# Kernel optimization log

Hardware: AMD Instinct MI355X
Metric: run time of the kernel (lower is better)

## Reference

```python
import jax, jax.numpy as jnp
import numpy as np

N_NODES = 100000
N_EDGES = 6400000


def setup_inputs() -> dict:
    key = jax.random.key(0)
    k = jax.random.split(key, 5)
    x = jax.random.normal(k[0], (N_NODES, 4), dtype=jnp.float32)
    edge_index = jax.random.randint(k[1], (2, N_EDGES), 0, N_NODES, dtype=jnp.int32)
    # Glorot-style init for GCN linear weights
    W1 = jax.random.normal(k[2], (4, 16), dtype=jnp.float32) * (1.0 / np.sqrt(4.0))
    b1 = jnp.zeros((16,), dtype=jnp.float32)
    W2 = jax.random.normal(k[3], (16, 2), dtype=jnp.float32) * (1.0 / np.sqrt(16.0))
    b2 = jnp.zeros((2,), dtype=jnp.float32)
    return {"x": x, "edge_index": edge_index, "W1": W1, "b1": b1, "W2": W2, "b2": b2}


def _gcn_conv(x, src, dst, deg_inv_sqrt, W, b):
    """One GCNConv layer: linear transform -> symmetric-normalized scatter-add -> bias.

    src, dst already include self-loops; deg_inv_sqrt precomputed on the
    self-loop-augmented graph (matches PyG GCNConv defaults).
    """
    n = x.shape[0]
    h = x @ W                                   # [N, F_out]
    coef = deg_inv_sqrt[src] * deg_inv_sqrt[dst]  # [E+N]
    msg = h[src] * coef[:, None]                # gather + scale, [E+N, F_out]
    out = jax.ops.segment_sum(msg, dst, num_segments=n)  # scatter-add
    return out + b


def reference(x, edge_index, W1, b1, W2, b2):
    n = x.shape[0]
    loop = jnp.arange(n, dtype=edge_index.dtype)
    src = jnp.concatenate([edge_index[0], loop])  # add self-loops
    dst = jnp.concatenate([edge_index[1], loop])
    deg = jax.ops.segment_sum(jnp.ones_like(dst, dtype=x.dtype), dst, num_segments=n)
    deg_inv_sqrt = jnp.where(deg > 0, jax.lax.rsqrt(deg), 0.0)

    h = jax.nn.relu(_gcn_conv(x, src, dst, deg_inv_sqrt, W1, b1))
    return _gcn_conv(h, src, dst, deg_inv_sqrt, W2, b2)
```

## Files before the change

kernel.cpp:

```cpp
#include <hip/hip_runtime.h>

#define TPB 256
#define CSH 10
#define CN 1024
#define NBC_MAX 128
#define STILE 8192
#define EPT (STILE / TPB)

#define P2 16
#define P2_SH 4
#define SB_SH 8
#define SBN_MAX 512

#define B20 1048576
#define S1F 131072.0f
#define S2F 8192.0f

typedef unsigned long long u64;

__device__ __forceinline__ unsigned enc_fx(float v, float scale) {
    int xi = __float2int_rn(v * scale);
    xi = max(-(B20 - 1), min(B20 - 1, xi));
    return (unsigned)(xi + B20);
}

__global__ void k_zero2(int* __restrict__ a, int na, int* __restrict__ b, int nb) {
    int i = blockIdx.x * blockDim.x + threadIdx.x;
    if (i < na) a[i] = 0;
    if (i < nb) b[i] = 0;
}

__global__ void k_hist0(const int* __restrict__ dst, int* __restrict__ hist0,
                        int NBC, int E) {
    __shared__ int hh[NBC_MAX];
    for (int i = threadIdx.x; i < NBC_MAX; i += TPB) hh[i] = 0;
    __syncthreads();
    int stride = gridDim.x * blockDim.x;
    for (int i = blockIdx.x * blockDim.x + threadIdx.x; i < E; i += stride)
        atomicAdd(&hh[dst[i] >> CSH], 1);
    __syncthreads();
    for (int i = threadIdx.x; i < NBC; i += TPB)
        if (hh[i]) atomicAdd(&hist0[i], hh[i]);
}

__global__ void k_scanbase(const int* __restrict__ bsize, int* __restrict__ base,
                           int* __restrict__ cur, int NBC) {
    __shared__ int s[NBC_MAX];
    int t = threadIdx.x;
    if (t < NBC_MAX) s[t] = (t < NBC) ? bsize[t] : 0;
    __syncthreads();
    for (int off = 1; off < NBC_MAX; off <<= 1) {
        int v = 0;
        if (t < NBC_MAX && t >= off) v = s[t - off];
        __syncthreads();
        if (t < NBC_MAX) s[t] += v;
        __syncthreads();
    }
    if (t < NBC) {
        int b = (t == 0) ? 0 : s[t - 1];
        base[t] = b;
        cur[t] = b;
    }
    if (t == 0) base[NBC] = s[NBC - 1];
}

__global__ void k_bscat(const int* __restrict__ src, const int* __restrict__ dst,
                        int* __restrict__ cur, unsigned* __restrict__ packed,
                        int E, int NBC) {
    __shared__ unsigned stage[STILE];
    __shared__ int cnt[NBC_MAX], lb[NBC_MAX], resv[NBC_MAX];
    int tb = blockIdx.x * STILE;
    int te = min(E, tb + STILE);
    if (threadIdx.x < NBC_MAX) cnt[threadIdx.x] = 0;
    __syncthreads();
    unsigned pk[EPT];
    int br[EPT];
#pragma unroll
    for (int u = 0; u < EPT; u++) {
        int i = tb + u * TPB + (int)threadIdx.x;
        br[u] = -1;
        if (i < te) {
            int d = dst[i];
            int b = d >> CSH;
            pk[u] = ((unsigned)src[i] << CSH) | (unsigned)(d & (CN - 1));
            int r = atomicAdd(&cnt[b], 1);
            br[u] = b | (r << 7);
        }
    }
    __syncthreads();
    if (threadIdx.x < (unsigned)NBC) {
        int b = threadIdx.x;
        int sum = 0;
        for (int j = 0; j < b; j++) sum += cnt[j];
        lb[b] = sum;
        resv[b] = cnt[b] ? atomicAdd(&cur[b], cnt[b]) : 0;
    }
    __syncthreads();
#pragma unroll
    for (int u = 0; u < EPT; u++) {
        if (br[u] >= 0) {
            int b = br[u] & (NBC_MAX - 1);
            stage[lb[b] + (br[u] >> 7)] = pk[u];
        }
    }
    __syncthreads();
    int wv = threadIdx.x >> 6, lane = threadIdx.x & 63;
    for (int b = wv; b < NBC; b += 4) {
        int c = cnt[b];
        if (!c) continue;
        int gb = resv[b], s0 = lb[b];
        for (int i = lane; i < c; i += 64)
            packed[gb + i] = stage[s0 + i];
    }
}

__global__ void k_p2hist(const unsigned* __restrict__ packed, const int* __restrict__ base,
                         int* __restrict__ h, int* __restrict__ deg, int SBN, int N) {
    __shared__ int hsb[SBN_MAX];
    __shared__ int dcnt[CN];
    int b = blockIdx.x >> P2_SH, p = blockIdx.x & (P2 - 1);
    for (int i = threadIdx.x; i < SBN_MAX; i += TPB) hsb[i] = 0;
    for (int i = threadIdx.x; i < CN; i += TPB) dcnt[i] = 0;
    __syncthreads();
    int lo = base[b], sz = base[b + 1] - lo;
    int i0 = lo + (int)((long long)sz * p / P2);
    int i1 = lo + (int)((long long)sz * (p + 1) / P2);
    int a0 = min(i1, (i0 + 3) & ~3);
    int a1 = a0 + ((i1 - a0) & ~3);
    for (int i = i0 + (int)threadIdx.x; i < a0; i += TPB) {
        unsigned pk = packed[i];
        atomicAdd(&hsb[pk >> (CSH + SB_SH)], 1);
        atomicAdd(&dcnt[pk & (CN - 1)], 1);
    }
    for (int i = a0 + (int)threadIdx.x * 4; i < a1; i += TPB * 4) {
        uint4 q = *(const uint4*)(packed + i);
        atomicAdd(&hsb[q.x >> (CSH + SB_SH)], 1); atomicAdd(&dcnt[q.x & (CN - 1)], 1);
        atomicAdd(&hsb[q.y >> (CSH + SB_SH)], 1); atomicAdd(&dcnt[q.y & (CN - 1)], 1);
        atomicAdd(&hsb[q.z >> (CSH + SB_SH)], 1); atomicAdd(&dcnt[q.z & (CN - 1)], 1);
        atomicAdd(&hsb[q.w >> (CSH + SB_SH)], 1); atomicAdd(&dcnt[q.w & (CN - 1)], 1);
    }
    for (int i = a1 + (int)threadIdx.x; i < i1; i += TPB) {
        unsigned pk = packed[i];
        atomicAdd(&hsb[pk >> (CSH + SB_SH)], 1);
        atomicAdd(&dcnt[pk & (CN - 1)], 1);
    }
    __syncthreads();
    int* hp = h + (size_t)blockIdx.x * SBN;
    for (int i2 = threadIdx.x; i2 < SBN; i2 += TPB) hp[i2] = hsb[i2];
    int node0 = b << CSH;
    for (int i2 = threadIdx.x; i2 < CN; i2 += TPB)
        if (dcnt[i2] && node0 + i2 < N) atomicAdd(&deg[node0 + i2], dcnt[i2]);
}

__global__ void k_scan3(int* __restrict__ h, const int* __restrict__ base, int SBN) {
    __shared__ int tsum[TPB];
    int b = blockIdx.x;
    int* hb = h + (size_t)b * P2 * SBN;
    int n = SBN * P2;
    int per = (n + TPB - 1) / TPB;
    int i0 = threadIdx.x * per;
    int vals[32];
    int sum = 0;
    for (int k = 0; k < per && k < 32; k++) {
        int idx = i0 + k;
        int v = 0;
        if (idx < n) {
            int sb = idx >> P2_SH, p = idx & (P2 - 1);
            v = hb[p * SBN + sb];
        }
        vals[k] = v;
        sum += v;
    }
    tsum[threadIdx.x] = sum;
    __syncthreads();
    for (int off = 1; off < TPB; off <<= 1) {
        int v = (threadIdx.x >= off) ? tsum[threadIdx.x - off] : 0;
        __syncthreads();
        tsum[threadIdx.x] += v;
        __syncthreads();
    }
    int run = base[b] + ((threadIdx.x == 0) ? 0 : tsum[threadIdx.x - 1]);
    for (int k = 0; k < per && k < 32; k++) {
        int idx = i0 + k;
        if (idx < n) {
            int sb = idx >> P2_SH, p = idx & (P2 - 1);
            hb[p * SBN + sb] = run;
            run += vals[k];
        }
    }
}

__global__ void k_p2scat(const unsigned* __restrict__ packed, const int* __restrict__ base,
                         const int* __restrict__ h, unsigned* __restrict__ packed2,
                         int SBN) {
    __shared__ int goff[SBN_MAX];
    __shared__ int cnt2[SBN_MAX];
    int b = blockIdx.x >> P2_SH, p = blockIdx.x & (P2 - 1);
    const int* hp = h + (size_t)blockIdx.x * SBN;
    for (int i = threadIdx.x; i < SBN_MAX; i += TPB) {
        cnt2[i] = 0;
        goff[i] = (i < SBN) ? hp[i] : 0;
    }
    __syncthreads();
    int lo = base[b], sz = base[b + 1] - lo;
    int i0 = lo + (int)((long long)sz * p / P2);
    int i1 = lo + (int)((long long)sz * (p + 1) / P2);
    int a0 = min(i1, (i0 + 3) & ~3);
    int a1 = a0 + ((i1 - a0) & ~3);
    for (int i = i0 + (int)threadIdx.x; i < a0; i += TPB) {
        unsigned pk = packed[i];
        int sb2 = pk >> (CSH + SB_SH);
        int r = atomicAdd(&cnt2[sb2], 1);
        packed2[goff[sb2] + r] = pk;
    }
    for (int i = a0 + (int)threadIdx.x * 4; i < a1; i += TPB * 4) {
        uint4 q = *(const uint4*)(packed + i);
        int sa = q.x >> (CSH + SB_SH), sb_ = q.y >> (CSH + SB_SH);
        int sc = q.z >> (CSH + SB_SH), sd = q.w >> (CSH + SB_SH);
        int ra = atomicAdd(&cnt2[sa], 1);
        int rb = atomicAdd(&cnt2[sb_], 1);
        int rc = atomicAdd(&cnt2[sc], 1);
        int rd = atomicAdd(&cnt2[sd], 1);
        packed2[goff[sa] + ra] = q.x;
        packed2[goff[sb_] + rb] = q.y;
        packed2[goff[sc] + rc] = q.z;
        packed2[goff[sd] + rd] = q.w;
    }
    for (int i = a1 + (int)threadIdx.x; i < i1; i += TPB) {
        unsigned pk = packed[i];
        int sb2 = pk >> (CSH + SB_SH);
        int r = atomicAdd(&cnt2[sb2], 1);
        packed2[goff[sb2] + r] = pk;
    }
}

__global__ void k_prepv(const float* __restrict__ x, const int* __restrict__ deg,
                        float* __restrict__ xs, unsigned* __restrict__ xse, int N) {
    int v = blockIdx.x * blockDim.x + threadIdx.x;
    if (v >= N) return;
    float di = rsqrtf((float)(deg[v] + 1));
    float4 xv = ((const float4*)x)[v];
    xv.x *= di; xv.y *= di; xv.z *= di; xv.w *= di;
    ((float4*)xs)[v] = xv;
    uint4 e;
    e.x = enc_fx(xv.x, S1F); e.y = enc_fx(xv.y, S1F);
    e.z = enc_fx(xv.z, S1F); e.w = enc_fx(xv.w, S1F);
    ((uint4*)xse)[v] = e;
}

#define AGG1_AT(pkv, gv) { int n_ = (int)((pkv) & (CN - 1)) * 3; \
    atomicAdd(&acc[n_],     (u64)(gv).x | ((u64)(gv).y << 32)); \
    atomicAdd(&acc[n_ + 1], (u64)(gv).z | ((u64)(gv).w << 32)); }

__global__ void k_agg1n(const unsigned* __restrict__ packed2, const int* __restrict__ base,
                        const unsigned* __restrict__ xse, u64* __restrict__ partial1, int S1) {
    __shared__ u64 acc[CN * 3];
    for (int i = threadIdx.x; i < CN * 3; i += TPB) acc[i] = 0ULL;
    __syncthreads();
    int b = blockIdx.x / S1, s = blockIdx.x - b * S1;
    int lo = base[b], sz = base[b + 1] - lo;
    int i0 = lo + (int)((long long)sz * s / S1);
    int i1 = lo + (int)((long long)sz * (s + 1) / S1);
    const uint4* xse4 = (const uint4*)xse;
    int i = i0 + (int)threadIdx.x;
    for (; i + 3 * TPB < i1; i += 4 * TPB) {
        unsigned pa = packed2[i];
        unsigned pb = packed2[i + TPB];
        unsigned pc = packed2[i + 2 * TPB];
        unsigned pd = packed2[i + 3 * TPB];
        uint4 ga = xse4[pa >> CSH];
        uint4 gb = xse4[pb >> CSH];
        uint4 gc = xse4[pc >> CSH];
        uint4 gd = xse4[pd >> CSH];
        AGG1_AT(pa, ga); AGG1_AT(pb, gb); AGG1_AT(pc, gc); AGG1_AT(pd, gd);
    }
    for (; i < i1; i += TPB) {
        unsigned pk = packed2[i];
        uint4 g = xse4[pk >> CSH];
        AGG1_AT(pk, g);
    }
    __syncthreads();
    u64* p = partial1 + (size_t)blockIdx.x * (CN * 2);
    for (int i2 = threadIdx.x; i2 < CN * 2; i2 += TPB)
        p[i2] = acc[(i2 >> 1) * 3 + (i2 & 1)];
}

__global__ void k_comb1q(const u64* __restrict__ partial1,
                         const float* __restrict__ xs, const int* __restrict__ deg,
                         const float* __restrict__ W1, const float* __restrict__ b1,
                         const float* __restrict__ W2,
                         float* __restrict__ hs2f, unsigned* __restrict__ hs2e,
                         int S1, int N) {
    __shared__ float w1[64], w2[32], bb[16];
    if (threadIdx.x < 64) w1[threadIdx.x] = W1[threadIdx.x];
    if (threadIdx.x < 32) w2[threadIdx.x] = W2[threadIdx.x];
    if (threadIdx.x < 16) bb[threadIdx.x] = b1[threadIdx.x];
    __syncthreads();
    int v = blockIdx.x * blockDim.x + threadIdx.x;
    if (v >= N) return;
    int b = v >> CSH, lv = v & (CN - 1);
    u64 a01 = 0, a23 = 0;
    for (int s = 0; s < S1; s++) {
        const u64* q = partial1 + ((size_t)(b * S1 + s) * CN + lv) * 2;
        a01 += q[0];
        a23 += q[1];
    }
    int dg = deg[v];
    long long bias = (long long)dg << 20;
    const float inv = 1.0f / S1F;
    float f0 = (float)((long long)(a01 & 0xffffffffULL) - bias) * inv;
    float f1 = (float)((long long)(a01 >> 32) - bias) * inv;
    float f2 = (float)((long long)(a23 & 0xffffffffULL) - bias) * inv;
    float f3 = (float)((long long)(a23 >> 32) - bias) * inv;
    float4 self = ((const float4*)xs)[v];
    float di = rsqrtf((float)(dg + 1));
    float v0 = (f0 + self.x) * di, v1 = (f1 + self.y) * di;
    float v2 = (f2 + self.z) * di, v3 = (f3 + self.w) * di;
    float s0 = 0.f, s1 = 0.f;
#pragma unroll
    for (int j = 0; j < 16; j++) {
        float h = v0 * w1[j] + v1 * w1[16 + j] + v2 * w1[32 + j] + v3 * w1[48 + j] + bb[j];
        h = fmaxf(h, 0.0f);
        s0 += h * w2[2 * j];
        s1 += h * w2[2 * j + 1];
    }
    s0 *= di; s1 *= di;
    ((float2*)hs2f)[v] = make_float2(s0, s1);
    uint2 e;
    e.x = enc_fx(s0, S2F);
    e.y = enc_fx(s1, S2F);
    ((uint2*)hs2e)[v] = e;
}

__global__ void k_agg2n(const unsigned* __restrict__ packed2, const int* __restrict__ base,
                        const unsigned* __restrict__ hs2e, u64* __restrict__ partial2, int S2) {
    __shared__ u64 acc[CN];
    for (int i = threadIdx.x; i < CN; i += TPB) acc[i] = 0ULL;
    __syncthreads();
    int b = blockIdx.x / S2, s = blockIdx.x - b * S2;
    int lo = base[b], sz = base[b + 1] - lo;
    int i0 = lo + (int)((long long)sz * s / S2);
    int i1 = lo + (int)((long long)sz * (s + 1) / S2);
    const uint2* h2 = (const uint2*)hs2e;
    int i = i0 + (int)threadIdx.x;
    for (; i + 3 * TPB < i1; i += 4 * TPB) {
        unsigned pa = packed2[i];
        unsigned pb = packed2[i + TPB];
        unsigned pc = packed2[i + 2 * TPB];
        unsigned pd = packed2[i + 3 * TPB];
        uint2 ga = h2[pa >> CSH];
        uint2 gb = h2[pb >> CSH];
        uint2 gc = h2[pc >> CSH];
        uint2 gd = h2[pd >> CSH];
        atomicAdd(&acc[pa & (CN - 1)], (u64)ga.x | ((u64)ga.y << 32));
        atomicAdd(&acc[pb & (CN - 1)], (u64)gb.x | ((u64)gb.y << 32));
        atomicAdd(&acc[pc & (CN - 1)], (u64)gc.x | ((u64)gc.y << 32));
        atomicAdd(&acc[pd & (CN - 1)], (u64)gd.x | ((u64)gd.y << 32));
    }
    for (; i < i1; i += TPB) {
        unsigned pk = packed2[i];
        uint2 g = h2[pk >> CSH];
        atomicAdd(&acc[pk & (CN - 1)], (u64)g.x | ((u64)g.y << 32));
    }
    __syncthreads();
    u64* p = partial2 + (size_t)blockIdx.x * CN;
    for (int i2 = threadIdx.x; i2 < CN; i2 += TPB) p[i2] = acc[i2];
}

__global__ void k_comb2q(const u64* __restrict__ partial2,
                         const float* __restrict__ hs2f, const int* __restrict__ deg,
                         const float* __restrict__ b2, float* __restrict__ out,
                         int S2, int N) {
    int v = blockIdx.x * blockDim.x + threadIdx.x;
    if (v >= N) return;
    int b = v >> CSH, lv = v & (CN - 1);
    u64 t = 0;
    for (int s = 0; s < S2; s++)
        t += partial2[(size_t)(b * S2 + s) * CN + lv];
    int dg = deg[v];
    long long bias = (long long)dg << 20;
    const float inv = 1.0f / S2F;
    float f0 = (float)((long long)(t & 0xffffffffULL) - bias) * inv;
    float f1 = (float)((long long)(t >> 32) - bias) * inv;
    float2 self = ((const float2*)hs2f)[v];
    float di = rsqrtf((float)(dg + 1));
    ((float2*)out)[v] = make_float2((f0 + self.x) * di + b2[0],
                                    (f1 + self.y) * di + b2[1]);
}


__global__ void k_zero(int* __restrict__ p, int n) {
    int i = blockIdx.x * blockDim.x + threadIdx.x;
    if (i < n) p[i] = 0;
}
__global__ void k_deg_fb(const int* __restrict__ dst, int* __restrict__ deg, int E) {
    int i = blockIdx.x * blockDim.x + threadIdx.x;
    if (i < E) atomicAdd(&deg[dst[i]], 1);
}
__global__ void k_dis_fb(const int* __restrict__ deg, float* __restrict__ dis, int N) {
    int v = blockIdx.x * blockDim.x + threadIdx.x;
    if (v < N) dis[v] = rsqrtf((float)(deg[v] + 1));
}
__global__ void k_lin1_fb(const float* __restrict__ x, const float* __restrict__ W1,
                          const float* __restrict__ dis, float* __restrict__ hs1,
                          float* __restrict__ agg1, int N) {
    __shared__ float w[64];
    if (threadIdx.x < 64) w[threadIdx.x] = W1[threadIdx.x];
    __syncthreads();
    int v = blockIdx.x * blockDim.x + threadIdx.x;
    if (v >= N) return;
    float4 xv = ((const float4*)x)[v];
    float d = dis[v];
#pragma unroll
    for (int j = 0; j < 16; j++) {
        float h = (xv.x * w[j] + xv.y * w[16 + j] + xv.z * w[32 + j] + xv.w * w[48 + j]) * d;
        hs1[v * 16 + j] = h;
        agg1[v * 16 + j] = h;
    }
}
__global__ void k_scat1_fb(const int* __restrict__ src, const int* __restrict__ dst,
                           const float* __restrict__ hs1, float* __restrict__ agg1, int E4) {
    int t = blockIdx.x * blockDim.x + threadIdx.x;
    if (t >= E4) return;
    int e = t >> 2, q = t & 3;
    int s = src[e], d = dst[e];
    float4 m = ((const float4*)hs1)[s * 4 + q];
    float* a = agg1 + (size_t)d * 16 + q * 4;
    atomicAdd(a + 0, m.x); atomicAdd(a + 1, m.y);
    atomicAdd(a + 2, m.z); atomicAdd(a + 3, m.w);
}
__global__ void k_lin2_fb(const float* __restrict__ agg1, const float* __restrict__ dis,
                          const float* __restrict__ b1, const float* __restrict__ W2,
                          float* __restrict__ hs2, float* __restrict__ agg2, int N) {
    __shared__ float w[32];
    __shared__ float bb[16];
    if (threadIdx.x < 32) w[threadIdx.x] = W2[threadIdx.x];
    if (threadIdx.x < 16) bb[threadIdx.x] = b1[threadIdx.x];
    __syncthreads();
    int v = blockIdx.x * blockDim.x + threadIdx.x;
    if (v >= N) return;
    float d = dis[v];
    float a0 = 0.f, a1 = 0.f;
#pragma unroll
    for (int k = 0; k < 16; k++) {
        float r = fmaxf(agg1[v * 16 + k] * d + bb[k], 0.0f);
        a0 += r * w[k * 2 + 0];
        a1 += r * w[k * 2 + 1];
    }
    float2 hv = make_float2(a0 * d, a1 * d);
    ((float2*)hs2)[v] = hv;
    ((float2*)agg2)[v] = hv;
}
__global__ void k_scat2_fb(const int* __restrict__ src, const int* __restrict__ dst,
                           const float* __restrict__ hs2, float* __restrict__ agg2, int E) {
    int e = blockIdx.x * blockDim.x + threadIdx.x;
    if (e >= E) return;
    int s = src[e], d = dst[e];
    float2 m = ((const float2*)hs2)[s];
    atomicAdd(&agg2[d * 2 + 0], m.x);
    atomicAdd(&agg2[d * 2 + 1], m.y);
}
__global__ void k_out_fb(const float* __restrict__ agg2, const float* __restrict__ dis,
                         const float* __restrict__ b2, float* __restrict__ out, int N) {
    int v = blockIdx.x * blockDim.x + threadIdx.x;
    if (v >= N) return;
    float d = dis[v];
    out[v * 2 + 0] = agg2[v * 2 + 0] * d + b2[0];
    out[v * 2 + 1] = agg2[v * 2 + 1] * d + b2[1];
}


extern "C" void kernel_launch(void* const* d_in, const int* in_sizes, int n_in,
                              void* d_out, int out_size, void* d_ws, size_t ws_size,
                              hipStream_t stream) {
    const float* x  = (const float*)d_in[0];
    const int*   ei = (const int*)d_in[1];
    const float* W1 = (const float*)d_in[2];
    const float* b1 = (const float*)d_in[3];
    const float* W2 = (const float*)d_in[4];
    const float* b2 = (const float*)d_in[5];

    const int N = in_sizes[0] / 4;
    const int E = in_sizes[1] / 2;
    const int* src = ei;
    const int* dst = ei + E;
    float* outp = (float*)d_out;

    auto align = [](size_t v) { return (v + 255) & ~(size_t)255; };
    const int NBC = (N + CN - 1) >> CSH;
    const int SBN = (N + (1 << SB_SH) - 1) >> SB_SH;
    const int NC  = NBC * P2 * SBN;
    const int gN  = (N + TPB - 1) / TPB;
    const int ntiles = (E + STILE - 1) / STILE;
    const bool src_fits = (size_t)N <= ((size_t)1 << (32 - CSH));
    const bool fx_safe = (long long)E <= (long long)N * 512;

    const int S1 = 16, S2 = 16;
    size_t part1_bytes = (size_t)NBC * S1 * CN * 16;
    size_t part2_bytes = (size_t)NBC * S2 * CN * 8;
    size_t pkA_bytes = (size_t)E * 4;
    if (part1_bytes > pkA_bytes) pkA_bytes = part1_bytes;
    if (part2_bytes > pkA_bytes) pkA_bytes = part2_bytes;

    size_t need_new = align(pkA_bytes)
                    + align((size_t)E * 4)
                    + align((size_t)N * 16)
                    + align((size_t)N * 16)
                    + align((size_t)N * 8)
                    + align((size_t)N * 8)
                    + align((size_t)N * 4)
                    + align((size_t)NC * 4)
                    + align((size_t)NBC * 4)
                    + align((size_t)NBC * 4)
                    + align((size_t)(NBC + 1) * 4);

    if (ws_size >= need_new && NBC <= NBC_MAX && SBN <= SBN_MAX && src_fits && fx_safe) {
        char* ws = (char*)d_ws;
        unsigned* packed = (unsigned*)ws;
        u64* partial1 = (u64*)ws;
        u64* partial2 = (u64*)ws;
        ws += align(pkA_bytes);
        unsigned* packed2 = (unsigned*)ws; ws += align((size_t)E * 4);
        float* xs    = (float*)ws;    ws += align((size_t)N * 16);
        unsigned* xse = (unsigned*)ws; ws += align((size_t)N * 16);
        float* hs2f  = (float*)ws;    ws += align((size_t)N * 8);
        unsigned* hs2e = (unsigned*)ws; ws += align((size_t)N * 8);
        int* deg     = (int*)ws;      ws += align((size_t)N * 4);
        int* h       = (int*)ws;      ws += align((size_t)NC * 4);
        int* hist0   = (int*)ws;      ws += align((size_t)NBC * 4);
        int* cur     = (int*)ws;      ws += align((size_t)NBC * 4);
        int* base    = (int*)ws;      ws += align((size_t)(NBC + 1) * 4);

        k_zero2<<<gN, TPB, 0, stream>>>(deg, N, hist0, NBC);
        k_hist0<<<1024, TPB, 0, stream>>>(dst, hist0, NBC, E);
        k_scanbase<<<1, TPB, 0, stream>>>(hist0, base, cur, NBC);
        k_bscat<<<ntiles, TPB, 0, stream>>>(src, dst, cur, packed, E, NBC);
        k_p2hist<<<NBC * P2, TPB, 0, stream>>>(packed, base, h, deg, SBN, N);
        k_scan3<<<NBC, TPB, 0, stream>>>(h, base, SBN);
        k_p2scat<<<NBC * P2, TPB, 0, stream>>>(packed, base, h, packed2, SBN);
        k_prepv<<<gN, TPB, 0, stream>>>(x, deg, xs, xse, N);
        k_agg1n<<<NBC * S1, TPB, 0, stream>>>(packed2, base, xse, partial1, S1);
        k_comb1q<<<gN, TPB, 0, stream>>>(partial1, xs, deg, W1, b1, W2, hs2f, hs2e, S1, N);
        k_agg2n<<<NBC * S2, TPB, 0, stream>>>(packed2, base, hs2e, partial2, S2);
        k_comb2q<<<gN, TPB, 0, stream>>>(partial2, hs2f, deg, b2, outp, S2, N);
    } else {
        char* ws = (char*)d_ws;
        int*   deg  = (int*)ws;   ws += align((size_t)N * 4);
        float* dis  = (float*)ws; ws += align((size_t)N * 4);
        float* hs1  = (float*)ws; ws += align((size_t)N * 16 * 4);
        float* agg1 = (float*)ws; ws += align((size_t)N * 16 * 4);
        float* hs2  = (float*)ws; ws += align((size_t)N * 2 * 4);
        float* agg2 = (float*)ws; ws += align((size_t)N * 2 * 4);
        int gE = (E + TPB - 1) / TPB;
        int gE4 = ((size_t)E * 4 + TPB - 1) / TPB;

        k_zero<<<gN, TPB, 0, stream>>>(deg, N);
        k_deg_fb<<<gE, TPB, 0, stream>>>(dst, deg, E);
        k_dis_fb<<<gN, TPB, 0, stream>>>(deg, dis, N);
        k_lin1_fb<<<gN, TPB, 0, stream>>>(x, W1, dis, hs1, agg1, N);
        k_scat1_fb<<<gE4, TPB, 0, stream>>>(src, dst, hs1, agg1, E * 4);
        k_lin2_fb<<<gN, TPB, 0, stream>>>(agg1, dis, b1, W2, hs2, agg2, N);
        k_scat2_fb<<<gE, TPB, 0, stream>>>(src, dst, hs2, agg2, E);
        k_out_fb<<<gN, TPB, 0, stream>>>(agg2, dis, b2, outp, N);
    }
}
```

Before: 271.1 us.

## Stage p2scat outputs in LDS bins and flush coalesced; vectorize hist0 loads

The second-pass scatter now buffers the first CAP entries of each sub-bucket in shared memory and writes them out contiguously per wavefront after a barrier, instead of issuing scattered 4-byte global stores. Entries beyond CAP still go directly to global memory. The destination histogram kernel reads dst with int4 loads, and the bucket-scatter tile size is halved. Using dynamic shared memory of SBN*(2+CAP) words may reduce occupancy, and the extra barrier and flush loop add work.

```diff
diff --git a/kernel.cpp b/kernel.cpp
--- a/kernel.cpp
+++ b/kernel.cpp
@@ -4,13 +4,14 @@
 #define CSH 10
 #define CN 1024
 #define NBC_MAX 128
-#define STILE 8192
+#define STILE 4096
 #define EPT (STILE / TPB)
 
 #define P2 16
 #define P2_SH 4
 #define SB_SH 8
 #define SBN_MAX 512
+#define CAP 20
 
 #define B20 1048576
 #define S1F 131072.0f
@@ -35,9 +36,19 @@
     __shared__ int hh[NBC_MAX];
     for (int i = threadIdx.x; i < NBC_MAX; i += TPB) hh[i] = 0;
     __syncthreads();
+    int E4 = E >> 2;
     int stride = gridDim.x * blockDim.x;
-    for (int i = blockIdx.x * blockDim.x + threadIdx.x; i < E; i += stride)
-        atomicAdd(&hh[dst[i] >> CSH], 1);
+    for (int i = blockIdx.x * blockDim.x + threadIdx.x; i < E4; i += stride) {
+        int4 d4 = ((const int4*)dst)[i];
+        atomicAdd(&hh[d4.x >> CSH], 1);
+        atomicAdd(&hh[d4.y >> CSH], 1);
+        atomicAdd(&hh[d4.z >> CSH], 1);
+        atomicAdd(&hh[d4.w >> CSH], 1);
+    }
+    if (blockIdx.x == 0) {
+        for (int i = (E4 << 2) + (int)threadIdx.x; i < E; i += TPB)
+            atomicAdd(&hh[dst[i] >> CSH], 1);
+    }
     __syncthreads();
     for (int i = threadIdx.x; i < NBC; i += TPB)
         if (hh[i]) atomicAdd(&hist0[i], hh[i]);
@@ -193,13 +204,15 @@
 __global__ void k_p2scat(const unsigned* __restrict__ packed, const int* __restrict__ base,
                          const int* __restrict__ h, unsigned* __restrict__ packed2,
                          int SBN) {
-    __shared__ int goff[SBN_MAX];
-    __shared__ int cnt2[SBN_MAX];
+    extern __shared__ int dsm[];
+    int* goff = dsm;
+    int* cnt2 = dsm + SBN;
+    unsigned* binbuf = (unsigned*)(dsm + 2 * SBN);
     int b = blockIdx.x >> P2_SH, p = blockIdx.x & (P2 - 1);
     const int* hp = h + (size_t)blockIdx.x * SBN;
-    for (int i = threadIdx.x; i < SBN_MAX; i += TPB) {
+    for (int i = threadIdx.x; i < SBN; i += TPB) {
         cnt2[i] = 0;
-        goff[i] = (i < SBN) ? hp[i] : 0;
+        goff[i] = hp[i];
     }
     __syncthreads();
     int lo = base[b], sz = base[b + 1] - lo;
@@ -211,7 +224,8 @@
         unsigned pk = packed[i];
         int sb2 = pk >> (CSH + SB_SH);
         int r = atomicAdd(&cnt2[sb2], 1);
-        packed2[goff[sb2] + r] = pk;
+        if (r < CAP) binbuf[sb2 * CAP + r] = pk;
+        else packed2[goff[sb2] + r] = pk;
     }
     for (int i = a0 + (int)threadIdx.x * 4; i < a1; i += TPB * 4) {
         uint4 q = *(const uint4*)(packed + i);
@@ -221,16 +235,26 @@
         int rb = atomicAdd(&cnt2[sb_], 1);
         int rc = atomicAdd(&cnt2[sc], 1);
         int rd = atomicAdd(&cnt2[sd], 1);
-        packed2[goff[sa] + ra] = q.x;
-        packed2[goff[sb_] + rb] = q.y;
-        packed2[goff[sc] + rc] = q.z;
-        packed2[goff[sd] + rd] = q.w;
+        if (ra < CAP) binbuf[sa * CAP + ra] = q.x; else packed2[goff[sa] + ra] = q.x;
+        if (rb < CAP) binbuf[sb_ * CAP + rb] = q.y; else packed2[goff[sb_] + rb] = q.y;
+        if (rc < CAP) binbuf[sc * CAP + rc] = q.z; else packed2[goff[sc] + rc] = q.z;
+        if (rd < CAP) binbuf[sd * CAP + rd] = q.w; else packed2[goff[sd] + rd] = q.w;
     }
     for (int i = a1 + (int)threadIdx.x; i < i1; i += TPB) {
         unsigned pk = packed[i];
         int sb2 = pk >> (CSH + SB_SH);
         int r = atomicAdd(&cnt2[sb2], 1);
-        packed2[goff[sb2] + r] = pk;
+        if (r < CAP) binbuf[sb2 * CAP + r] = pk;
+        else packed2[goff[sb2] + r] = pk;
+    }
+    __syncthreads();
+    int wv = threadIdx.x >> 6, lane = threadIdx.x & 63;
+    for (int sb2 = wv; sb2 < SBN; sb2 += 4) {
+        int c = min(cnt2[sb2], CAP);
+        if (!c) continue;
+        int gb = goff[sb2];
+        for (int i = lane; i < c; i += 64)
+            packed2[gb + i] = binbuf[sb2 * CAP + i];
     }
 }
 
@@ -514,6 +538,8 @@
                     + align((size_t)NBC * 4)
                     + align((size_t)(NBC + 1) * 4);
 
+    const size_t p2s_smem = (size_t)SBN * (2 + CAP) * 4;
+
     if (ws_size >= need_new && NBC <= NBC_MAX && SBN <= SBN_MAX && src_fits && fx_safe) {
         char* ws = (char*)d_ws;
         unsigned* packed = (unsigned*)ws;
@@ -537,7 +563,7 @@
         k_bscat<<<ntiles, TPB, 0, stream>>>(src, dst, cur, packed, E, NBC);
         k_p2hist<<<NBC * P2, TPB, 0, stream>>>(packed, base, h, deg, SBN, N);
         k_scan3<<<NBC, TPB, 0, stream>>>(h, base, SBN);
-        k_p2scat<<<NBC * P2, TPB, 0, stream>>>(packed, base, h, packed2, SBN);
+        k_p2scat<<<NBC * P2, TPB, p2s_smem, stream>>>(packed, base, h, packed2, SBN);
         k_prepv<<<gN, TPB, 0, stream>>>(x, deg, xs, xse, N);
         k_agg1n<<<NBC * S1, TPB, 0, stream>>>(packed2, base, xse, partial1, S1);
         k_comb1q<<<gN, TPB, 0, stream>>>(partial1, xs, deg, W1, b1, W2, hs2f, hs2e, S1, N);
```

Result: faster. 258.4 us (-4.7%).
